# Optimization experiments

Measured on AMD Instinct MI355X. Metric: run time of the kernel, lower is better.

The kernel has to match this reference:

```python
import jax, jax.numpy as jnp
import numpy as np

B, WIN = 2048, 11          # batch, hardcoded window_size=11
K, VOCAB = 4096, 30522     # hash dim, bert-base-uncased vocab
NOUT, TOPK = 18, 64        # action logits, top-k active hash bits
THRESH = 1e-10


def setup_inputs() -> dict:
    key = jax.random.key(0)
    k1, k2, k3 = jax.random.split(key, 3)
    # avoid id 0 (padding) so sentence_lengths > 0
    ids = jax.random.randint(k1, (B, 1, WIN), 1, VOCAB, dtype=jnp.int32)
    W = jax.random.normal(k2, (K, VOCAB, 2), dtype=jnp.float32)  # view_as_complex layout
    w_out = jax.random.normal(k3, (NOUT, K), dtype=jnp.float32) * 0.02
    b_out = jnp.zeros((NOUT,), dtype=jnp.float32)
    return {"ids": ids, "W": W, "w_out": w_out, "b_out": b_out}


def reference(ids, W, w_out, b_out):
    ids2 = ids.reshape(ids.shape[0], ids.shape[-1])
    nz = (ids2 != 0)
    position_ids = jnp.cumsum(nz, axis=-1)
    sl = nz.sum(-1)
    sl = jnp.where(sl > 0, sl, ids2.shape[-1])                   # fallback branch
    pos = jnp.pi * position_ids / sl[:, None].astype(jnp.float32)
    o_re, o_im = jnp.cos(pos), jnp.sin(pos)

    Wre, Wim = W[..., 0], W[..., 1]                              # complex W parts [K, V]
    g_re = jnp.take(Wre, ids2, axis=1)
    g_im = jnp.take(Wim, ids2, axis=1)
    W_abs = jnp.sqrt(g_re * g_re + g_im * g_im)

    # phis = W_indices * conj(one_roots): (a+bi)(c-di)
    p_re = g_re * o_re + g_im * o_im
    p_im = g_im * o_re - g_re * o_im
    # clamp tiny real/imag components to +THRESH (matches torch r_phis edit)
    p_re = jnp.where((p_re < THRESH) & (p_re > -THRESH), THRESH, p_re)
    p_im = jnp.where((p_im < THRESH) & (p_im > -THRESH), THRESH, p_im)
    ang = jnp.abs(jnp.arctan2(p_im, p_re))

    phi_factor = (W_abs + ang) * nz                              # added_factors=True
    pf = phi_factor.sum(-1).T                                    # [B, K]

    # argsort descending, take top k, scatter True -> binary hash
    _, idx = jax.lax.top_k(pf, TOPK)                             # [B, TOPK]
    rows = jnp.arange(pf.shape[0])[:, None]
    feat = jnp.zeros_like(pf).at[rows, idx].set(1.0)             # [B, K] float

    logits = feat @ w_out.T + b_out                              # [B, NOUT]
    return logits
```

## Files before the change

kernel.cpp:

```cpp
#include <hip/hip_runtime.h>
#include <hip/hip_bf16.h>
#include <stdint.h>

#define B_     2048
#define WIN_   11
#define K_     4096
#define VOCAB_ 30522
#define NOUT_  18
#define TOPK_  64
#define NPAIR_ (B_ * WIN_)
#define PI_F   3.14159274101257324f

#define NCH_    15
#define CHUNK_  2048
#define UNITS_  1024
#define UPK_    15261
#define TAILU_  925
#define KPB_    16
#define NBLK_   (K_ / KPB_)
#define GTOT_   (NCH_ * KPB_)
#define PFTH_   1024
#define PROD_   512
#define CONS_   512
#define PCON_BYTES_ (NPAIR_ * 4)
#define SMEM_BYTES_ (PCON_BYTES_ + 4 * CHUNK_ * 8)

static_assert(GTOT_ % 4 == 0, "unroll-4 rotation");

__global__ void prep_kernel(const int* __restrict__ ids, float2* __restrict__ ocs) {
    int b = blockIdx.x * blockDim.x + threadIdx.x;
    if (b >= B_) return;
    const int* row = ids + b * WIN_;
    int poss[WIN_];
    int cnt = 0;
#pragma unroll
    for (int w = 0; w < WIN_; ++w) { cnt += (row[w] != 0); poss[w] = cnt; }
    float fsl = (float)((cnt > 0) ? cnt : WIN_);
#pragma unroll
    for (int w = 0; w < WIN_; ++w) {
        float pos = __fdiv_rn(__fmul_rn(PI_F, (float)poss[w]), fsl);
        float2 o;
        o.x = cosf(pos);
        o.y = sinf(pos);
        ocs[b * WIN_ + w] = o;
    }
}

__global__ __launch_bounds__(512) void bucket_kernel(const int* __restrict__ ids,
                                                     const float2* __restrict__ ocs,
                                                     float4* __restrict__ smeta,
                                                     int* __restrict__ chunkstart) {
    __shared__ int lcnt[512 * NCH_];
    __shared__ int segtot[NCH_][8];
    __shared__ int tot[NCH_];
    __shared__ int bbase[NCH_ + 1];
    const int t = threadIdx.x;

#pragma unroll
    for (int c = 0; c < NCH_; ++c) lcnt[t * NCH_ + c] = 0;
    __syncthreads();

    for (int p = t; p < NPAIR_; p += 512) {
        int id = ids[p];
        if (id != 0) lcnt[t * NCH_ + (id / CHUNK_)] += 1;
    }
    __syncthreads();

    if (t < NCH_ * 8) {
        int bkt = t >> 3, seg = t & 7;
        int run = 0;
        for (int i = 0; i < 64; ++i) {
            int idx = (seg * 64 + i) * NCH_ + bkt;
            int tmp = lcnt[idx];
            lcnt[idx] = run;
            run += tmp;
        }
        segtot[bkt][seg] = run;
    }
    __syncthreads();
    if (t < NCH_) {
        int run = 0;
#pragma unroll
        for (int s = 0; s < 8; ++s) { int tmp = segtot[t][s]; segtot[t][s] = run; run += tmp; }
        tot[t] = run;
    }
    __syncthreads();
    if (t == 0) {
        int run = 0;
#pragma unroll
        for (int c = 0; c < NCH_; ++c) { bbase[c] = run; run += tot[c]; }
        bbase[NCH_] = run;
#pragma unroll
        for (int c = 0; c <= NCH_; ++c) chunkstart[c] = bbase[c];
    }
    __syncthreads();
    if (t < NCH_ * 8) {
        int bkt = t >> 3, seg = t & 7;
        int add = segtot[bkt][seg];
        for (int i = 0; i < 64; ++i) lcnt[(seg * 64 + i) * NCH_ + bkt] += add;
    }
    __syncthreads();

    for (int p = t; p < NPAIR_; p += 512) {
        int id = ids[p];
        if (id == 0) continue;
        int bkt = id / CHUNK_;
        int pos = bbase[bkt] + lcnt[t * NCH_ + bkt];
        lcnt[t * NCH_ + bkt] += 1;
        float2 o = ocs[p];
        float4 m;
        m.x = __int_as_float(id);
        m.y = __int_as_float(p);
        m.z = o.x;
        m.w = o.y;
        smeta[pos] = m;
    }
}

__device__ __forceinline__ void pair_body(const float4 m, const float2* __restrict__ sb,
                                          int lo, float* __restrict__ pcontrib) {
    int id  = __float_as_int(m.x);
    int dst = __float_as_int(m.y);
    float2 g = sb[id - lo];
    float wabs = sqrtf(__fadd_rn(__fmul_rn(g.x, g.x), __fmul_rn(g.y, g.y)));
    float pre = __fadd_rn(__fmul_rn(g.x, m.z), __fmul_rn(g.y, m.w));
    float pim = __fsub_rn(__fmul_rn(g.y, m.z), __fmul_rn(g.x, m.w));
    if (pre < 1e-10f && pre > -1e-10f) pre = 1e-10f;
    if (pim < 1e-10f && pim > -1e-10f) pim = 1e-10f;
    float ang = fabsf(atan2f(pim, pre));
    pcontrib[dst] = __fadd_rn(wabs, ang);
}

__global__ __launch_bounds__(PFTH_, 1) void pf_kernel(const float4* __restrict__ W4,
                                                      const float4* __restrict__ smeta,
                                                      const int* __restrict__ chunkstart,
                                                      float* __restrict__ pfT) {
    extern __shared__ char smem[];
    float*  pcontrib = (float*)smem;
    char*   sbuf     = smem + PCON_BYTES_;
    __shared__ int cstart[NCH_ + 1];

    const int t = threadIdx.x;
    const int kbase = blockIdx.x * KPB_;
    const float4* Wb = W4 + (size_t)kbase * UPK_;

    if (t <= NCH_) cstart[t] = chunkstart[t];
    __syncthreads();

    float4 p0a, p0b, p1a, p1b, p2a, p2b, p3a, p3b;
    float4 A0{}, A1{}, A2{}, B0{}, B1{}, B2{};

    {
        ((float4*)sbuf)[t] = Wb[t];
        if (t < PROD_) {
            p1a = Wb[1 * UNITS_ + t];  p1b = Wb[1 * UNITS_ + PROD_ + t];
            p2a = Wb[2 * UNITS_ + t];  p2b = Wb[2 * UNITS_ + PROD_ + t];
            p3a = Wb[3 * UNITS_ + t];  p3b = Wb[3 * UNITS_ + PROD_ + t];
        } else {
            int ct = t - PROD_;
            int q0 = ct;               if (q0 > NPAIR_ - 1) q0 = NPAIR_ - 1;
            int q1 = CONS_ + ct;       if (q1 > NPAIR_ - 1) q1 = NPAIR_ - 1;
            int q2 = 2 * CONS_ + ct;   if (q2 > NPAIR_ - 1) q2 = NPAIR_ - 1;
            A0 = smeta[q0]; A1 = smeta[q1]; A2 = smeta[q2];
        }
        for (int i = t; i < NPAIR_; i += PFTH_) pcontrib[i] = 0.0f;
    }
    asm volatile("s_waitcnt vmcnt(0) lgkmcnt(0)" ::: "memory");
    __builtin_amdgcn_s_barrier();
    __builtin_amdgcn_sched_barrier(0);

#define PHASE(J, LDa, LDb, WRa, WRb, SU0, SU1, SU2, SL0, SL1, SL2)               \
    {                                                                            \
        const int p_ = g + (J);                                                  \
        __builtin_amdgcn_sched_barrier(0);                                       \
        asm volatile("s_waitcnt lgkmcnt(0)" ::: "memory");                       \
        __builtin_amdgcn_s_barrier();                                            \
        __builtin_amdgcn_sched_barrier(0);                                       \
        int ccj_ = cc + (J); int kkj_ = kk;                                      \
        if (ccj_ >= NCH_) { ccj_ -= NCH_; kkj_ += 1; }                           \
        if (t < PROD_) {                                                         \
                           \
            if (p_ + 1 < GTOT_) {                                                \
                int cwc_ = ccj_ + 1; if (cwc_ >= NCH_) cwc_ = 0;                 \
                int nw_ = (cwc_ == NCH_ - 1) ? TAILU_ : UNITS_;                  \
                float4* dstb_ = (float4*)(sbuf + (size_t)((p_ + 1) & 3) * (CHUNK_ * 8)); \
                if (t < nw_)         dstb_[t] = WRa;                             \
                if (PROD_ + t < nw_) dstb_[PROD_ + t] = WRb;                     \
            }                                                                    \
                                             \
            {   int cl_ = ccj_ + 4; int kl_ = kkj_;                              \
                if (cl_ >= NCH_) { cl_ -= NCH_; kl_ += 1; }                      \
                if (p_ + 4 >= GTOT_) { cl_ = NCH_ - 1; kl_ = KPB_ - 1; }         \
                int nu_ = (cl_ == NCH_ - 1) ? TAILU_ : UNITS_;                   \
                const float4* src_ = W4 + (size_t)(kbase + kl_) * UPK_ + (size_t)cl_ * UNITS_; \
                if (t < nu_)         LDa = src_[t];                              \
                if (PROD_ + t < nu_) LDb = src_[PROD_ + t];                      \
            }                                                                    \
        } else {                                                                 \
            int ct_ = t - PROD_;                                                 \
                                               \
            {   int cn_ = ccj_ + 1; if (cn_ >= NCH_) cn_ = 0;                    \
                int ns_ = cstart[cn_];                                           \
                int q0_ = ns_ + ct_;             if (q0_ > NPAIR_ - 1) q0_ = NPAIR_ - 1; \
                int q1_ = ns_ + CONS_ + ct_;     if (q1_ > NPAIR_ - 1) q1_ = NPAIR_ - 1; \
                int q2_ = ns_ + 2 * CONS_ + ct_; if (q2_ > NPAIR_ - 1) q2_ = NPAIR_ - 1; \
                SL0 = smeta[q0_]; SL1 = smeta[q1_]; SL2 = smeta[q2_]; }          \
                                                            \
            {   const float2* sb_ = (const float2*)(sbuf + (size_t)(p_ & 3) * (CHUNK_ * 8)); \
                const int lo_ = ccj_ * CHUNK_;                                   \
                const int cs_ = cstart[ccj_], ce_ = cstart[ccj_ + 1];            \
                if (cs_ + ct_ < ce_)             pair_body(SU0, sb_, lo_, pcontrib); \
                if (cs_ + CONS_ + ct_ < ce_)     pair_body(SU1, sb_, lo_, pcontrib); \
                if (cs_ + 2 * CONS_ + ct_ < ce_) pair_body(SU2, sb_, lo_, pcontrib); \
                for (int pp_ = cs_ + 3 * CONS_ + ct_; pp_ < ce_; pp_ += CONS_)   \
                    pair_body(smeta[pp_], sb_, lo_, pcontrib); }                 \
        }                                                                        \
             \
        if (ccj_ == NCH_ - 1) {                                                  \
            __builtin_amdgcn_sched_barrier(0);                                   \
            asm volatile("s_waitcnt lgkmcnt(0)" ::: "memory");                   \
            __builtin_amdgcn_s_barrier();                                        \
            __builtin_amdgcn_sched_barrier(0);                                   \
            float* outp_ = pfT + (size_t)(kbase + kkj_) * B_;                    \
            _Pragma("unroll")                                                    \
            for (int i_ = 0; i_ < B_ / PFTH_; ++i_) {                            \
                int b_ = i_ * PFTH_ + t;                                         \
                float acc_ = 0.0f;                                               \
                _Pragma("unroll")                                                \
                for (int w_ = 0; w_ < WIN_; ++w_)                                \
                    acc_ = __fadd_rn(acc_, pcontrib[b_ * WIN_ + w_]);            \
                outp_[b_] = acc_;                                                \
            }                                                                    \
        }                                                                        \
    }

#pragma unroll 1
    for (int g = 0; g < GTOT_; g += 4) {
        const int cc = g % NCH_, kk = g / NCH_;
        PHASE(0, p0a, p0b, p1a, p1b, A0, A1, A2, B0, B1, B2)
        PHASE(1, p1a, p1b, p2a, p2b, B0, B1, B2, A0, A1, A2)
        PHASE(2, p2a, p2b, p3a, p3b, A0, A1, A2, B0, B1, B2)
        PHASE(3, p3a, p3b, p0a, p0b, B0, B1, B2, A0, A1, A2)
    }
#undef PHASE
}

__global__ __launch_bounds__(256) void transpose_kb(const float* __restrict__ pfT,
                                                    float* __restrict__ pf) {
    __shared__ float tile[64][65];
    int kb = blockIdx.x * 64;
    int bb = blockIdx.y * 64;
    int tx = threadIdx.x & 63;
    int ty = threadIdx.x >> 6;
#pragma unroll
    for (int i = 0; i < 64; i += 4)
        tile[ty + i][tx] = pfT[(size_t)(kb + ty + i) * B_ + (bb + tx)];
    __syncthreads();
#pragma unroll
    for (int i = 0; i < 64; i += 4)
        pf[(size_t)(bb + ty + i) * K_ + (kb + tx)] = tile[tx][ty + i];
}

__global__ __launch_bounds__(256) void topk_logits_kernel(const float* __restrict__ pf,
                                                          const float* __restrict__ w_out,
                                                          const float* __restrict__ b_out,
                                                          float* __restrict__ out) {
    const int b = blockIdx.x;
    const int t = threadIdx.x;
    __shared__ uint32_t srow[K_];
    __shared__ int hist[256];
    __shared__ int sfx[256];
    __shared__ uint32_t sh_prefix;
    __shared__ int sh_need;
    __shared__ int wave_gt[4], wave_eq[4];
    __shared__ int gt_running, eq_running;
    __shared__ int idxlist[TOPK_];
    __shared__ float partial[4][NOUT_];

    const float* rowp = pf + (size_t)b * K_;
    for (int i = t; i < K_; i += 256) srow[i] = __float_as_uint(rowp[i]);
    if (t == 0) { sh_prefix = 0u; sh_need = TOPK_; gt_running = 0; eq_running = 0; }
    __syncthreads();

    for (int pass = 0; pass < 4; ++pass) {
        int shift = 24 - 8 * pass;
        uint32_t himask = (pass == 0) ? 0u : (0xFFFFFFFFu << (shift + 8));
        hist[t] = 0;
        __syncthreads();
        uint32_t prefix = sh_prefix & himask;
        for (int i = t; i < K_; i += 256) {
            uint32_t u = srow[i];
            if ((u & himask) == prefix) atomicAdd(&hist[(u >> shift) & 255], 1);
        }
        __syncthreads();
        sfx[t] = hist[t];
        __syncthreads();
#pragma unroll
        for (int off = 1; off < 256; off <<= 1) {
            int v = (t + off < 256) ? sfx[t + off] : 0;
            __syncthreads();
            sfx[t] += v;
            __syncthreads();
        }
        int need = sh_need;
        int above = (t == 255) ? 0 : sfx[t + 1];
        if (sfx[t] >= need && above < need) {
            sh_prefix |= ((uint32_t)t << shift);
            sh_need = need - above;
        }
        __syncthreads();
    }
    const uint32_t T = sh_prefix;
    const int r = sh_need;
    const int c_gt = TOPK_ - r;

    for (int cbase = 0; cbase < K_; cbase += 256) {
        uint32_t u = srow[cbase + t];
        bool gt = (u > T);
        bool eq = (u == T);
        unsigned long long mg = __ballot(gt);
        unsigned long long me = __ballot(eq);
        int lane = t & 63, wv = t >> 6;
        if (lane == 0) { wave_gt[wv] = __popcll(mg); wave_eq[wv] = __popcll(me); }
        __syncthreads();
        int offg = gt_running, offe = eq_running;
        for (int w2 = 0; w2 < wv; ++w2) { offg += wave_gt[w2]; offe += wave_eq[w2]; }
        unsigned long long lmask = (lane == 0) ? 0ull : ((~0ull) >> (64 - lane));
        int rkg = offg + __popcll(mg & lmask);
        int rke = offe + __popcll(me & lmask);
        if (gt) idxlist[rkg] = cbase + t;
        else if (eq && rke < r) idxlist[c_gt + rke] = cbase + t;
        __syncthreads();
        if (t == 0) {
            gt_running += wave_gt[0] + wave_gt[1] + wave_gt[2] + wave_gt[3];
            eq_running += wave_eq[0] + wave_eq[1] + wave_eq[2] + wave_eq[3];
        }
        __syncthreads();
    }

    {
        int lane = t & 63, wv4 = t >> 6;
        if (lane < NOUT_) {
            const float* wrow = w_out + (size_t)lane * K_;
            float s = 0.0f;
#pragma unroll
            for (int j = 0; j < TOPK_ / 4; ++j) s += wrow[idxlist[wv4 * (TOPK_ / 4) + j]];
            partial[wv4][lane] = s;
        }
        __syncthreads();
        if (t < NOUT_) {
            float s = b_out[t] + partial[0][t] + partial[1][t] + partial[2][t] + partial[3][t];
            out[b * NOUT_ + t] = s;
        }
    }
}

extern "C" void kernel_launch(void* const* d_in, const int* in_sizes, int n_in,
                              void* d_out, int out_size, void* d_ws, size_t ws_size,
                              hipStream_t stream) {
    const int*   ids   = (const int*)d_in[0];
    const float* W     = (const float*)d_in[1];
    const float* w_out = (const float*)d_in[2];
    const float* b_out = (const float*)d_in[3];
    float* out = (float*)d_out;

    char* ws = (char*)d_ws;
    const size_t pf_bytes = (size_t)K_ * B_ * sizeof(float);
    float*  pfT   = (float*)(ws);
    float*  pf    = (float*)(ws + pf_bytes);
    float2* ocs   = (float2*)(ws + 2 * pf_bytes);
    float4* smeta = (float4*)(ws + 2 * pf_bytes + 256 * 1024);
    int* chunkstart = (int*)(ws + 2 * pf_bytes + 768 * 1024);

    (void)hipFuncSetAttribute((const void*)pf_kernel,
                              hipFuncAttributeMaxDynamicSharedMemorySize,
                              SMEM_BYTES_);

    prep_kernel<<<(B_ + 255) / 256, 256, 0, stream>>>(ids, ocs);
    bucket_kernel<<<1, 512, 0, stream>>>(ids, ocs, smeta, chunkstart);
    pf_kernel<<<NBLK_, PFTH_, SMEM_BYTES_, stream>>>((const float4*)W, smeta, chunkstart, pfT);
    transpose_kb<<<dim3(K_ / 64, B_ / 64), 256, 0, stream>>>(pfT, pf);
    topk_logits_kernel<<<B_, 256, 0, stream>>>(pf, w_out, b_out, out);
}
```

Measured before the change: 410.2 us.

## Replace block-wide barriers with LDS flag-based producer/consumer warp specialization

Swaps the lockstep barrier-per-phase pipeline for warp-specialized producers (4 waves) and consumers (12 waves) that signal each other through LDS counters and spin-waits with s_sleep. Producers stage W chunks into a 4-deep ring buffer as soon as consumers release a slot. Consumers process pairs as soon as a chunk is ready, so the two roles are decoupled and consumers get more threads. The cost is spin-wait overhead and LDS atomics, a risk of stalls or deadlock if the memory ordering assumptions fail, and fewer waves issuing global loads.

```diff
diff --git a/kernel.cpp b/kernel.cpp
--- a/kernel.cpp
+++ b/kernel.cpp
@@ -20,12 +20,12 @@
 #define NBLK_   (K_ / KPB_)
 #define GTOT_   (NCH_ * KPB_)
 #define PFTH_   1024
-#define PROD_   512
-#define CONS_   512
+#define PRT_    256
+#define CNT_    768
+#define NPW_    4
+#define NCW_    12
 #define PCON_BYTES_ (NPAIR_ * 4)
 #define SMEM_BYTES_ (PCON_BYTES_ + 4 * CHUNK_ * 8)
-
-static_assert(GTOT_ % 4 == 0, "unroll-4 rotation");
 
 __global__ void prep_kernel(const int* __restrict__ ids, float2* __restrict__ ocs) {
     int b = blockIdx.x * blockDim.x + threadIdx.x;
@@ -136,113 +136,113 @@
                                                       const int* __restrict__ chunkstart,
                                                       float* __restrict__ pfT) {
     extern __shared__ char smem[];
-    float*  pcontrib = (float*)smem;
-    char*   sbuf     = smem + PCON_BYTES_;
+    float* pcontrib = (float*)smem;
+    char*  sbuf     = smem + PCON_BYTES_;
     __shared__ int cstart[NCH_ + 1];
+    __shared__ int ready_[4];
+    __shared__ int prodcnt_[4];
+    __shared__ int done_[4];
+    __shared__ int kcnt_;
+    __shared__ int sumcnt_;
 
     const int t = threadIdx.x;
     const int kbase = blockIdx.x * KPB_;
-    const float4* Wb = W4 + (size_t)kbase * UPK_;
 
     if (t <= NCH_) cstart[t] = chunkstart[t];
-    __syncthreads();
-
-    float4 p0a, p0b, p1a, p1b, p2a, p2b, p3a, p3b;
-    float4 A0{}, A1{}, A2{}, B0{}, B1{}, B2{};
-
-    {
-        ((float4*)sbuf)[t] = Wb[t];
-        if (t < PROD_) {
-            p1a = Wb[1 * UNITS_ + t];  p1b = Wb[1 * UNITS_ + PROD_ + t];
-            p2a = Wb[2 * UNITS_ + t];  p2b = Wb[2 * UNITS_ + PROD_ + t];
-            p3a = Wb[3 * UNITS_ + t];  p3b = Wb[3 * UNITS_ + PROD_ + t];
-        } else {
-            int ct = t - PROD_;
-            int q0 = ct;               if (q0 > NPAIR_ - 1) q0 = NPAIR_ - 1;
-            int q1 = CONS_ + ct;       if (q1 > NPAIR_ - 1) q1 = NPAIR_ - 1;
-            int q2 = 2 * CONS_ + ct;   if (q2 > NPAIR_ - 1) q2 = NPAIR_ - 1;
-            A0 = smeta[q0]; A1 = smeta[q1]; A2 = smeta[q2];
-        }
-        for (int i = t; i < NPAIR_; i += PFTH_) pcontrib[i] = 0.0f;
-    }
-    asm volatile("s_waitcnt vmcnt(0) lgkmcnt(0)" ::: "memory");
-    __builtin_amdgcn_s_barrier();
-    __builtin_amdgcn_sched_barrier(0);
-
-#define PHASE(J, LDa, LDb, WRa, WRb, SU0, SU1, SU2, SL0, SL1, SL2)               \
-    {                                                                            \
-        const int p_ = g + (J);                                                  \
-        __builtin_amdgcn_sched_barrier(0);                                       \
+    if (t < 4) { ready_[t] = 0; prodcnt_[t] = 0; done_[t] = 0; }
+    if (t == 4) { kcnt_ = 0; }
+    if (t == 5) { sumcnt_ = 0; }
+    for (int i = t; i < NPAIR_; i += PFTH_) pcontrib[i] = 0.0f;
+    __syncthreads();
+
+#define LOADCH(GP, R0, R1, R2, R3)                                               \
+    {   int g2_ = (GP);                                                          \
+        if (g2_ < GTOT_) {                                                       \
+            int kk2_ = g2_ / NCH_, cc2_ = g2_ % NCH_;                            \
+            int nu2_ = (cc2_ == NCH_ - 1) ? TAILU_ : UNITS_;                     \
+            const float4* src2_ = W4 + (size_t)(kbase + kk2_) * UPK_ + (size_t)cc2_ * UNITS_; \
+            if (t < nu2_)            R0 = src2_[t];                              \
+            if (PRT_ + t < nu2_)     R1 = src2_[PRT_ + t];                       \
+            if (2 * PRT_ + t < nu2_) R2 = src2_[2 * PRT_ + t];                   \
+            if (3 * PRT_ + t < nu2_) R3 = src2_[3 * PRT_ + t];                   \
+        }                                                                        \
+    }
+
+#define PSTEP(GP, R0, R1, R2, R3)                                                \
+    {   const int g_ = (GP);                                                     \
+        const int b_ = g_ & 3, u_ = g_ >> 2;                                     \
+        const int cc_ = g_ % NCH_;                                               \
+        const int nu_ = (cc_ == NCH_ - 1) ? TAILU_ : UNITS_;                     \
+        while (*(volatile int*)&done_[b_] < u_ * NCW_) __builtin_amdgcn_s_sleep(1); \
+        asm volatile("" ::: "memory");                                           \
+        float4* dst_ = (float4*)(sbuf + (size_t)b_ * (CHUNK_ * 8));              \
+        if (t < nu_)            dst_[t] = R0;                                    \
+        if (PRT_ + t < nu_)     dst_[PRT_ + t] = R1;                             \
+        if (2 * PRT_ + t < nu_) dst_[2 * PRT_ + t] = R2;                         \
+        if (3 * PRT_ + t < nu_) dst_[3 * PRT_ + t] = R3;                         \
         asm volatile("s_waitcnt lgkmcnt(0)" ::: "memory");                       \
-        __builtin_amdgcn_s_barrier();                                            \
-        __builtin_amdgcn_sched_barrier(0);                                       \
-        int ccj_ = cc + (J); int kkj_ = kk;                                      \
-        if (ccj_ >= NCH_) { ccj_ -= NCH_; kkj_ += 1; }                           \
-        if (t < PROD_) {                                                         \
-                           \
-            if (p_ + 1 < GTOT_) {                                                \
-                int cwc_ = ccj_ + 1; if (cwc_ >= NCH_) cwc_ = 0;                 \
-                int nw_ = (cwc_ == NCH_ - 1) ? TAILU_ : UNITS_;                  \
-                float4* dstb_ = (float4*)(sbuf + (size_t)((p_ + 1) & 3) * (CHUNK_ * 8)); \
-                if (t < nw_)         dstb_[t] = WRa;                             \
-                if (PROD_ + t < nw_) dstb_[PROD_ + t] = WRb;                     \
-            }                                                                    \
-                                             \
-            {   int cl_ = ccj_ + 4; int kl_ = kkj_;                              \
-                if (cl_ >= NCH_) { cl_ -= NCH_; kl_ += 1; }                      \
-                if (p_ + 4 >= GTOT_) { cl_ = NCH_ - 1; kl_ = KPB_ - 1; }         \
-                int nu_ = (cl_ == NCH_ - 1) ? TAILU_ : UNITS_;                   \
-                const float4* src_ = W4 + (size_t)(kbase + kl_) * UPK_ + (size_t)cl_ * UNITS_; \
-                if (t < nu_)         LDa = src_[t];                              \
-                if (PROD_ + t < nu_) LDb = src_[PROD_ + t];                      \
-            }                                                                    \
-        } else {                                                                 \
-            int ct_ = t - PROD_;                                                 \
-                                               \
-            {   int cn_ = ccj_ + 1; if (cn_ >= NCH_) cn_ = 0;                    \
-                int ns_ = cstart[cn_];                                           \
-                int q0_ = ns_ + ct_;             if (q0_ > NPAIR_ - 1) q0_ = NPAIR_ - 1; \
-                int q1_ = ns_ + CONS_ + ct_;     if (q1_ > NPAIR_ - 1) q1_ = NPAIR_ - 1; \
-                int q2_ = ns_ + 2 * CONS_ + ct_; if (q2_ > NPAIR_ - 1) q2_ = NPAIR_ - 1; \
-                SL0 = smeta[q0_]; SL1 = smeta[q1_]; SL2 = smeta[q2_]; }          \
-                                                            \
-            {   const float2* sb_ = (const float2*)(sbuf + (size_t)(p_ & 3) * (CHUNK_ * 8)); \
-                const int lo_ = ccj_ * CHUNK_;                                   \
-                const int cs_ = cstart[ccj_], ce_ = cstart[ccj_ + 1];            \
-                if (cs_ + ct_ < ce_)             pair_body(SU0, sb_, lo_, pcontrib); \
-                if (cs_ + CONS_ + ct_ < ce_)     pair_body(SU1, sb_, lo_, pcontrib); \
-                if (cs_ + 2 * CONS_ + ct_ < ce_) pair_body(SU2, sb_, lo_, pcontrib); \
-                for (int pp_ = cs_ + 3 * CONS_ + ct_; pp_ < ce_; pp_ += CONS_)   \
-                    pair_body(smeta[pp_], sb_, lo_, pcontrib); }                 \
-        }                                                                        \
-             \
-        if (ccj_ == NCH_ - 1) {                                                  \
-            __builtin_amdgcn_sched_barrier(0);                                   \
-            asm volatile("s_waitcnt lgkmcnt(0)" ::: "memory");                   \
-            __builtin_amdgcn_s_barrier();                                        \
-            __builtin_amdgcn_sched_barrier(0);                                   \
-            float* outp_ = pfT + (size_t)(kbase + kkj_) * B_;                    \
-            _Pragma("unroll")                                                    \
-            for (int i_ = 0; i_ < B_ / PFTH_; ++i_) {                            \
-                int b_ = i_ * PFTH_ + t;                                         \
-                float acc_ = 0.0f;                                               \
-                _Pragma("unroll")                                                \
-                for (int w_ = 0; w_ < WIN_; ++w_)                                \
-                    acc_ = __fadd_rn(acc_, pcontrib[b_ * WIN_ + w_]);            \
-                outp_[b_] = acc_;                                                \
+        if ((t & 63) == 0) {                                                     \
+            int old_ = atomicAdd(&prodcnt_[b_], 1);                              \
+            if (old_ == u_ * NPW_ + (NPW_ - 1)) {                                \
+                asm volatile("s_waitcnt lgkmcnt(0)" ::: "memory");               \
+                *(volatile int*)&ready_[b_] = g_ + 1;                            \
             }                                                                    \
         }                                                                        \
-    }
-
+        LOADCH(g_ + 4, R0, R1, R2, R3)                                           \
+    }
+
+    if (t < PRT_) {
+        float4 a0, a1, a2, a3, b0, b1, b2, b3, c0, c1, c2, c3, d0, d1, d2, d3;
+        LOADCH(0, a0, a1, a2, a3)
+        LOADCH(1, b0, b1, b2, b3)
+        LOADCH(2, c0, c1, c2, c3)
+        LOADCH(3, d0, d1, d2, d3)
 #pragma unroll 1
-    for (int g = 0; g < GTOT_; g += 4) {
-        const int cc = g % NCH_, kk = g / NCH_;
-        PHASE(0, p0a, p0b, p1a, p1b, A0, A1, A2, B0, B1, B2)
-        PHASE(1, p1a, p1b, p2a, p2b, B0, B1, B2, A0, A1, A2)
-        PHASE(2, p2a, p2b, p3a, p3b, A0, A1, A2, B0, B1, B2)
-        PHASE(3, p3a, p3b, p0a, p0b, B0, B1, B2, A0, A1, A2)
-    }
-#undef PHASE
+        for (int g = 0; g < GTOT_; g += 4) {
+            PSTEP(g + 0, a0, a1, a2, a3)
+            PSTEP(g + 1, b0, b1, b2, b3)
+            PSTEP(g + 2, c0, c1, c2, c3)
+            PSTEP(g + 3, d0, d1, d2, d3)
+        }
+    } else {
+        const int ct = t - PRT_;
+        int cc = 0, kk = 0;
+#pragma unroll 1
+        for (int g = 0; g < GTOT_; ++g) {
+            const int b = g & 3;
+            while (*(volatile int*)&ready_[b] < g + 1) __builtin_amdgcn_s_sleep(1);
+            asm volatile("" ::: "memory");
+            const float2* sb = (const float2*)(sbuf + (size_t)b * (CHUNK_ * 8));
+            const int lo = cc * CHUNK_;
+            const int cs = cstart[cc], ce = cstart[cc + 1];
+            for (int p = cs + ct; p < ce; p += CNT_)
+                pair_body(smeta[p], sb, lo, pcontrib);
+            asm volatile("s_waitcnt lgkmcnt(0)" ::: "memory");
+            if ((t & 63) == 0) atomicAdd(&done_[b], 1);
+            if (cc == NCH_ - 1) {
+                if ((t & 63) == 0) atomicAdd(&kcnt_, 1);
+                while (*(volatile int*)&kcnt_ < (kk + 1) * NCW_) __builtin_amdgcn_s_sleep(1);
+                asm volatile("" ::: "memory");
+                float* outp = pfT + (size_t)(kbase + kk) * B_;
+                for (int bb = ct; bb < B_; bb += CNT_) {
+                    float acc = 0.0f;
+#pragma unroll
+                    for (int w = 0; w < WIN_; ++w)
+                        acc = __fadd_rn(acc, pcontrib[bb * WIN_ + w]);
+                    outp[bb] = acc;
+                }
+                asm volatile("s_waitcnt lgkmcnt(0)" ::: "memory");
+                if ((t & 63) == 0) atomicAdd(&sumcnt_, 1);
+                while (*(volatile int*)&sumcnt_ < (kk + 1) * NCW_) __builtin_amdgcn_s_sleep(1);
+                asm volatile("" ::: "memory");
+                cc = 0; ++kk;
+            } else {
+                ++cc;
+            }
+        }
+    }
+#undef PSTEP
+#undef LOADCH
 }
 
 __global__ __launch_bounds__(256) void transpose_kb(const float* __restrict__ pfT,
```

Measured after the change: 575.9 us. 1.4x slower.

## Rebalance producer/consumer warps, compress pair metadata, use shared trig table

Applied to the files above, without the earlier changes.

Moves the pf_kernel split from 512 producer / 512 consumer threads to 256 producer / 768 consumer threads. Producers now hold four register loads per chunk with nontemporal hints, and more threads are available for the atan2-heavy pair work. Per-pair metadata shrinks from float4 to int2 by packing a trig-table index into the upper bits of the destination index, with the 121 possible cos/sin values computed once per block in shared memory. This cuts metadata traffic and consumer register use, at the cost of more producer registers and an extra LDS lookup per pair.

```diff
diff --git a/kernel.cpp b/kernel.cpp
--- a/kernel.cpp
+++ b/kernel.cpp
@@ -20,14 +20,16 @@
 #define NBLK_   (K_ / KPB_)
 #define GTOT_   (NCH_ * KPB_)
 #define PFTH_   1024
-#define PROD_   512
-#define CONS_   512
+#define PRT_    256
+#define CNT_    768
 #define PCON_BYTES_ (NPAIR_ * 4)
 #define SMEM_BYTES_ (PCON_BYTES_ + 4 * CHUNK_ * 8)
 
 static_assert(GTOT_ % 4 == 0, "unroll-4 rotation");
 
-__global__ void prep_kernel(const int* __restrict__ ids, float2* __restrict__ ocs) {
+typedef float vf4 __attribute__((ext_vector_type(4)));
+
+__global__ void prep_kernel(const int* __restrict__ ids, int* __restrict__ tabv) {
     int b = blockIdx.x * blockDim.x + threadIdx.x;
     if (b >= B_) return;
     const int* row = ids + b * WIN_;
@@ -35,20 +37,18 @@
     int cnt = 0;
 #pragma unroll
     for (int w = 0; w < WIN_; ++w) { cnt += (row[w] != 0); poss[w] = cnt; }
-    float fsl = (float)((cnt > 0) ? cnt : WIN_);
+    int sl = (cnt > 0) ? cnt : WIN_;
 #pragma unroll
     for (int w = 0; w < WIN_; ++w) {
-        float pos = __fdiv_rn(__fmul_rn(PI_F, (float)poss[w]), fsl);
-        float2 o;
-        o.x = cosf(pos);
-        o.y = sinf(pos);
-        ocs[b * WIN_ + w] = o;
+        int tb = (poss[w] - 1) * 11 + (sl - 1);
+        if (tb < 0) tb = 0;
+        tabv[b * WIN_ + w] = tb;
     }
 }
 
 __global__ __launch_bounds__(512) void bucket_kernel(const int* __restrict__ ids,
-                                                     const float2* __restrict__ ocs,
-                                                     float4* __restrict__ smeta,
+                                                     const int* __restrict__ tabv,
+                                                     int2* __restrict__ smeta,
                                                      int* __restrict__ chunkstart) {
     __shared__ int lcnt[512 * NCH_];
     __shared__ int segtot[NCH_][8];
@@ -107,69 +107,86 @@
         int bkt = id / CHUNK_;
         int pos = bbase[bkt] + lcnt[t * NCH_ + bkt];
         lcnt[t * NCH_ + bkt] += 1;
-        float2 o = ocs[p];
-        float4 m;
-        m.x = __int_as_float(id);
-        m.y = __int_as_float(p);
-        m.z = o.x;
-        m.w = o.y;
-        smeta[pos] = m;
-    }
-}
-
-__device__ __forceinline__ void pair_body(const float4 m, const float2* __restrict__ sb,
-                                          int lo, float* __restrict__ pcontrib) {
-    int id  = __float_as_int(m.x);
-    int dst = __float_as_int(m.y);
+        int2 mm;
+        mm.x = id;
+        mm.y = p | (tabv[p] << 16);
+        smeta[pos] = mm;
+    }
+}
+
+__device__ __forceinline__ void pair_body2(const int2 m, const float2* __restrict__ sb,
+                                           int lo, const float2* __restrict__ trig,
+                                           float* __restrict__ pcontrib) {
+    int id  = m.x;
+    int dst = m.y & 0xFFFF;
+    int tab = m.y >> 16;
+    float2 o = trig[tab];
     float2 g = sb[id - lo];
     float wabs = sqrtf(__fadd_rn(__fmul_rn(g.x, g.x), __fmul_rn(g.y, g.y)));
-    float pre = __fadd_rn(__fmul_rn(g.x, m.z), __fmul_rn(g.y, m.w));
-    float pim = __fsub_rn(__fmul_rn(g.y, m.z), __fmul_rn(g.x, m.w));
+    float pre = __fadd_rn(__fmul_rn(g.x, o.x), __fmul_rn(g.y, o.y));
+    float pim = __fsub_rn(__fmul_rn(g.y, o.x), __fmul_rn(g.x, o.y));
     if (pre < 1e-10f && pre > -1e-10f) pre = 1e-10f;
     if (pim < 1e-10f && pim > -1e-10f) pim = 1e-10f;
     float ang = fabsf(atan2f(pim, pre));
     pcontrib[dst] = __fadd_rn(wabs, ang);
 }
 
-__global__ __launch_bounds__(PFTH_, 1) void pf_kernel(const float4* __restrict__ W4,
-                                                      const float4* __restrict__ smeta,
+__global__ __launch_bounds__(PFTH_, 1) void pf_kernel(const vf4* __restrict__ W4,
+                                                      const int2* __restrict__ smeta,
                                                       const int* __restrict__ chunkstart,
                                                       float* __restrict__ pfT) {
     extern __shared__ char smem[];
-    float*  pcontrib = (float*)smem;
-    char*   sbuf     = smem + PCON_BYTES_;
+    float* pcontrib = (float*)smem;
+    char*  sbuf     = smem + PCON_BYTES_;
     __shared__ int cstart[NCH_ + 1];
+    __shared__ float2 trigS[121];
 
     const int t = threadIdx.x;
     const int kbase = blockIdx.x * KPB_;
-    const float4* Wb = W4 + (size_t)kbase * UPK_;
 
     if (t <= NCH_) cstart[t] = chunkstart[t];
-    __syncthreads();
-
-    float4 p0a, p0b, p1a, p1b, p2a, p2b, p3a, p3b;
-    float4 A0{}, A1{}, A2{}, B0{}, B1{}, B2{};
-
-    {
-        ((float4*)sbuf)[t] = Wb[t];
-        if (t < PROD_) {
-            p1a = Wb[1 * UNITS_ + t];  p1b = Wb[1 * UNITS_ + PROD_ + t];
-            p2a = Wb[2 * UNITS_ + t];  p2b = Wb[2 * UNITS_ + PROD_ + t];
-            p3a = Wb[3 * UNITS_ + t];  p3b = Wb[3 * UNITS_ + PROD_ + t];
-        } else {
-            int ct = t - PROD_;
-            int q0 = ct;               if (q0 > NPAIR_ - 1) q0 = NPAIR_ - 1;
-            int q1 = CONS_ + ct;       if (q1 > NPAIR_ - 1) q1 = NPAIR_ - 1;
-            int q2 = 2 * CONS_ + ct;   if (q2 > NPAIR_ - 1) q2 = NPAIR_ - 1;
-            A0 = smeta[q0]; A1 = smeta[q1]; A2 = smeta[q2];
-        }
-        for (int i = t; i < NPAIR_; i += PFTH_) pcontrib[i] = 0.0f;
-    }
+    if (t < 121) {
+        int pp = t / 11 + 1, ss = t % 11 + 1;
+        float pos = __fdiv_rn(__fmul_rn(PI_F, (float)pp), (float)ss);
+        trigS[t] = make_float2(cosf(pos), sinf(pos));
+    }
+
+#define LOADCH(GP, R0, R1, R2, R3)                                               \
+    {   int g2_ = (GP);                                                          \
+        if (g2_ < GTOT_) {                                                       \
+            int kk2_ = g2_ / NCH_, cc2_ = g2_ % NCH_;                            \
+            int nu2_ = (cc2_ == NCH_ - 1) ? TAILU_ : UNITS_;                     \
+            const vf4* s2_ = W4 + (size_t)(kbase + kk2_) * UPK_ + (size_t)cc2_ * UNITS_; \
+            if (t < nu2_)            R0 = __builtin_nontemporal_load(&s2_[t]);   \
+            if (PRT_ + t < nu2_)     R1 = __builtin_nontemporal_load(&s2_[PRT_ + t]); \
+            if (2 * PRT_ + t < nu2_) R2 = __builtin_nontemporal_load(&s2_[2 * PRT_ + t]); \
+            if (3 * PRT_ + t < nu2_) R3 = __builtin_nontemporal_load(&s2_[3 * PRT_ + t]); \
+        }                                                                        \
+    }
+
+    vf4 a0, a1, a2, a3, b0, b1, b2, b3, c0, c1, c2, c3, d0, d1, d2, d3;
+    int2 A0{}, A1{}, B0{}, B1{};
+
+    if (t < PRT_) {
+        LOADCH(0, a0, a1, a2, a3)
+        {   vf4* db = (vf4*)sbuf;
+            db[t] = a0; db[PRT_ + t] = a1;
+            db[2 * PRT_ + t] = a2; db[3 * PRT_ + t] = a3; }
+        LOADCH(1, b0, b1, b2, b3)
+        LOADCH(2, c0, c1, c2, c3)
+        LOADCH(3, d0, d1, d2, d3)
+    } else {
+        int ct = t - PRT_;
+        int q0 = ct;         if (q0 > NPAIR_ - 1) q0 = NPAIR_ - 1;
+        int q1 = CNT_ + ct;  if (q1 > NPAIR_ - 1) q1 = NPAIR_ - 1;
+        A0 = smeta[q0]; A1 = smeta[q1];
+    }
+    for (int i = t; i < NPAIR_; i += PFTH_) pcontrib[i] = 0.0f;
     asm volatile("s_waitcnt vmcnt(0) lgkmcnt(0)" ::: "memory");
     __builtin_amdgcn_s_barrier();
     __builtin_amdgcn_sched_barrier(0);
 
-#define PHASE(J, LDa, LDb, WRa, WRb, SU0, SU1, SU2, SL0, SL1, SL2)               \
+#define PHASE(J, L0, L1, L2, L3, Wr0, Wr1, Wr2, Wr3, SU0, SU1, SL0, SL1)         \
     {                                                                            \
         const int p_ = g + (J);                                                  \
         __builtin_amdgcn_sched_barrier(0);                                       \
@@ -178,44 +195,32 @@
         __builtin_amdgcn_sched_barrier(0);                                       \
         int ccj_ = cc + (J); int kkj_ = kk;                                      \
         if (ccj_ >= NCH_) { ccj_ -= NCH_; kkj_ += 1; }                           \
-        if (t < PROD_) {                                                         \
-                           \
+        if (t < PRT_) {                                                          \
             if (p_ + 1 < GTOT_) {                                                \
-                int cwc_ = ccj_ + 1; if (cwc_ >= NCH_) cwc_ = 0;                 \
-                int nw_ = (cwc_ == NCH_ - 1) ? TAILU_ : UNITS_;                  \
-                float4* dstb_ = (float4*)(sbuf + (size_t)((p_ + 1) & 3) * (CHUNK_ * 8)); \
-                if (t < nw_)         dstb_[t] = WRa;                             \
-                if (PROD_ + t < nw_) dstb_[PROD_ + t] = WRb;                     \
+                int cw_ = ccj_ + 1; if (cw_ >= NCH_) cw_ = 0;                    \
+                int nw_ = (cw_ == NCH_ - 1) ? TAILU_ : UNITS_;                   \
+                vf4* db_ = (vf4*)(sbuf + (size_t)((p_ + 1) & 3) * (CHUNK_ * 8)); \
+                if (t < nw_)            db_[t] = Wr0;                            \
+                if (PRT_ + t < nw_)     db_[PRT_ + t] = Wr1;                     \
+                if (2 * PRT_ + t < nw_) db_[2 * PRT_ + t] = Wr2;                 \
+                if (3 * PRT_ + t < nw_) db_[3 * PRT_ + t] = Wr3;                 \
             }                                                                    \
-                                             \
-            {   int cl_ = ccj_ + 4; int kl_ = kkj_;                              \
-                if (cl_ >= NCH_) { cl_ -= NCH_; kl_ += 1; }                      \
-                if (p_ + 4 >= GTOT_) { cl_ = NCH_ - 1; kl_ = KPB_ - 1; }         \
-                int nu_ = (cl_ == NCH_ - 1) ? TAILU_ : UNITS_;                   \
-                const float4* src_ = W4 + (size_t)(kbase + kl_) * UPK_ + (size_t)cl_ * UNITS_; \
-                if (t < nu_)         LDa = src_[t];                              \
-                if (PROD_ + t < nu_) LDb = src_[PROD_ + t];                      \
-            }                                                                    \
+            LOADCH(p_ + 4, L0, L1, L2, L3)                                       \
         } else {                                                                 \
-            int ct_ = t - PROD_;                                                 \
-                                               \
+            const int ct_ = t - PRT_;                                            \
             {   int cn_ = ccj_ + 1; if (cn_ >= NCH_) cn_ = 0;                    \
                 int ns_ = cstart[cn_];                                           \
-                int q0_ = ns_ + ct_;             if (q0_ > NPAIR_ - 1) q0_ = NPAIR_ - 1; \
-                int q1_ = ns_ + CONS_ + ct_;     if (q1_ > NPAIR_ - 1) q1_ = NPAIR_ - 1; \
-                int q2_ = ns_ + 2 * CONS_ + ct_; if (q2_ > NPAIR_ - 1) q2_ = NPAIR_ - 1; \
-                SL0 = smeta[q0_]; SL1 = smeta[q1_]; SL2 = smeta[q2_]; }          \
-                                                            \
+                int q0_ = ns_ + ct_;         if (q0_ > NPAIR_ - 1) q0_ = NPAIR_ - 1; \
+                int q1_ = ns_ + CNT_ + ct_;  if (q1_ > NPAIR_ - 1) q1_ = NPAIR_ - 1; \
+                SL0 = smeta[q0_]; SL1 = smeta[q1_]; }                            \
             {   const float2* sb_ = (const float2*)(sbuf + (size_t)(p_ & 3) * (CHUNK_ * 8)); \
                 const int lo_ = ccj_ * CHUNK_;                                   \
                 const int cs_ = cstart[ccj_], ce_ = cstart[ccj_ + 1];            \
-                if (cs_ + ct_ < ce_)             pair_body(SU0, sb_, lo_, pcontrib); \
-                if (cs_ + CONS_ + ct_ < ce_)     pair_body(SU1, sb_, lo_, pcontrib); \
-                if (cs_ + 2 * CONS_ + ct_ < ce_) pair_body(SU2, sb_, lo_, pcontrib); \
-                for (int pp_ = cs_ + 3 * CONS_ + ct_; pp_ < ce_; pp_ += CONS_)   \
-                    pair_body(smeta[pp_], sb_, lo_, pcontrib); }                 \
+                if (cs_ + ct_ < ce_)        pair_body2(SU0, sb_, lo_, trigS, pcontrib); \
+                if (cs_ + CNT_ + ct_ < ce_) pair_body2(SU1, sb_, lo_, trigS, pcontrib); \
+                for (int pp_ = cs_ + 2 * CNT_ + ct_; pp_ < ce_; pp_ += CNT_)     \
+                    pair_body2(smeta[pp_], sb_, lo_, trigS, pcontrib); }         \
         }                                                                        \
-             \
         if (ccj_ == NCH_ - 1) {                                                  \
             __builtin_amdgcn_sched_barrier(0);                                   \
             asm volatile("s_waitcnt lgkmcnt(0)" ::: "memory");                   \
@@ -237,12 +242,13 @@
 #pragma unroll 1
     for (int g = 0; g < GTOT_; g += 4) {
         const int cc = g % NCH_, kk = g / NCH_;
-        PHASE(0, p0a, p0b, p1a, p1b, A0, A1, A2, B0, B1, B2)
-        PHASE(1, p1a, p1b, p2a, p2b, B0, B1, B2, A0, A1, A2)
-        PHASE(2, p2a, p2b, p3a, p3b, A0, A1, A2, B0, B1, B2)
-        PHASE(3, p3a, p3b, p0a, p0b, B0, B1, B2, A0, A1, A2)
+        PHASE(0, a0, a1, a2, a3, b0, b1, b2, b3, A0, A1, B0, B1)
+        PHASE(1, b0, b1, b2, b3, c0, c1, c2, c3, B0, B1, A0, A1)
+        PHASE(2, c0, c1, c2, c3, d0, d1, d2, d3, A0, A1, B0, B1)
+        PHASE(3, d0, d1, d2, d3, a0, a1, a2, a3, B0, B1, A0, A1)
     }
 #undef PHASE
+#undef LOADCH
 }
 
 __global__ __launch_bounds__(256) void transpose_kb(const float* __restrict__ pfT,
@@ -366,19 +372,19 @@
 
     char* ws = (char*)d_ws;
     const size_t pf_bytes = (size_t)K_ * B_ * sizeof(float);
-    float*  pfT   = (float*)(ws);
-    float*  pf    = (float*)(ws + pf_bytes);
-    float2* ocs   = (float2*)(ws + 2 * pf_bytes);
-    float4* smeta = (float4*)(ws + 2 * pf_bytes + 256 * 1024);
+    float* pfT   = (float*)(ws);
+    float* pf    = (float*)(ws + pf_bytes);
+    int*   tabv  = (int*)(ws + 2 * pf_bytes);
+    int2*  smeta = (int2*)(ws + 2 * pf_bytes + 256 * 1024);
     int* chunkstart = (int*)(ws + 2 * pf_bytes + 768 * 1024);
 
     (void)hipFuncSetAttribute((const void*)pf_kernel,
                               hipFuncAttributeMaxDynamicSharedMemorySize,
                               SMEM_BYTES_);
 
-    prep_kernel<<<(B_ + 255) / 256, 256, 0, stream>>>(ids, ocs);
-    bucket_kernel<<<1, 512, 0, stream>>>(ids, ocs, smeta, chunkstart);
-    pf_kernel<<<NBLK_, PFTH_, SMEM_BYTES_, stream>>>((const float4*)W, smeta, chunkstart, pfT);
+    prep_kernel<<<(B_ + 255) / 256, 256, 0, stream>>>(ids, tabv);
+    bucket_kernel<<<1, 512, 0, stream>>>(ids, tabv, smeta, chunkstart);
+    pf_kernel<<<NBLK_, PFTH_, SMEM_BYTES_, stream>>>((const vf4*)W, smeta, chunkstart, pfT);
     transpose_kb<<<dim3(K_ / 64, B_ / 64), 256, 0, stream>>>(pfT, pf);
     topk_logits_kernel<<<B_, 256, 0, stream>>>(pf, w_out, b_out, out);
 }
```

Measured after the change: 404.5 us. Within noise of the previous version (-1.4%).
